# Kernel tuning notes

Hardware: AMD Instinct MI355X
Metric: run time of the kernel (lower is better)

Reference implementation:

```python
import jax, jax.numpy as jnp
import numpy as np


def setup_inputs() -> dict:
    key = jax.random.key(0)
    k1, k2 = jax.random.split(key)
    n_tokens, hidden, n_experts = 16384, 3072, 64
    activations = jax.random.normal(k1, (n_tokens, hidden), dtype=jnp.float32)
    logits = jax.random.normal(k2, (n_tokens, n_experts), dtype=jnp.float32)
    capacity = 256  # int(capacity_factor * n_tokens / n_experts) with capacity_factor=1.0
    return {"activations": activations, "logits": logits, "capacity": capacity}


def reference(activations, logits, capacity):
    """Top-1 MoE gating + capacity-limited token dispatch (DeepSpeed MoEGating, top_k=1).

    Returns (moe_input, scores, expert_assignment, mapped_slots, expert_counts).
    Dispatched rows are pre-scaled by the gate score (fused scale-and-scatter).
    """
    n_tokens, hidden = activations.shape
    n_experts = logits.shape[1]

    probs = jax.nn.softmax(logits, axis=-1)                       # [T, E], fp32
    expert = jnp.argmax(logits, axis=-1)                          # [T]
    mask1 = jax.nn.one_hot(expert, n_experts, dtype=jnp.int32)    # [T, E]

    # position of each token within its chosen expert's allocation
    locations = jnp.cumsum(mask1, axis=0) - 1                     # [T, E]
    loc_s = jnp.sum(locations * mask1, axis=1)                    # [T]

    keep = loc_s < capacity                                       # capacity-based dropping
    score = jnp.take_along_axis(probs, expert[:, None], axis=1)[:, 0]
    score = jnp.where(keep, score, 0.0)

    # dispatch buffer size, padded to a multiple of 256 (matches kernel path)
    size = n_experts * capacity
    if size % 256 != 0:
        size = size + (256 - size % 256)

    slots = expert * capacity + loc_s                             # [T]
    slots_scatter = jnp.where(keep, slots, size)                  # OOB index -> dropped

    moe_input = jnp.zeros((size, hidden), dtype=activations.dtype)
    moe_input = moe_input.at[slots_scatter].set(
        activations * score[:, None].astype(activations.dtype), mode="drop")

    expert_assignment = expert.astype(jnp.int32)
    mapped_slots = jnp.where(keep, slots, -1).astype(jnp.int32)
    expert_counts = jnp.sum(mask1 * keep[:, None].astype(jnp.int32), axis=0).astype(jnp.int32)

    return moe_input, score, expert_assignment, mapped_slots, expert_counts
```

## Files before the change

kernel.cpp:

```cpp
#include <hip/hip_runtime.h>

#define T_TOKENS 16384
#define HIDDEN   3072
#define NEXP     64
#define CAP      256
#define BLK      256
#define NGB      (T_TOKENS / BLK)
#define DSIZE    (NEXP * CAP)

__global__ __launch_bounds__(BLK) void gate_kernel(
    const float* __restrict__ logits,
    int* __restrict__ expertOut, int* __restrict__ rankOut,
    float* __restrict__ scoreOut, int* __restrict__ blockCounts) {
  __shared__ int eLds[BLK];
  __shared__ int hist[NEXP];

  const int t = blockIdx.x * BLK + threadIdx.x;

  const float4* lg = (const float4*)(logits + (size_t)t * NEXP);
  float l[NEXP];
#pragma unroll
  for (int i = 0; i < NEXP / 4; ++i) {
    float4 v = lg[i];
    l[4 * i + 0] = v.x; l[4 * i + 1] = v.y;
    l[4 * i + 2] = v.z; l[4 * i + 3] = v.w;
  }

  float mx = l[0];
  int arg = 0;
#pragma unroll
  for (int i = 1; i < NEXP; ++i) {
    if (l[i] > mx) { mx = l[i]; arg = i; }
  }
  float s = 0.f;
#pragma unroll
  for (int i = 0; i < NEXP; ++i) s += __expf(l[i] - mx);
  const float score = 1.0f / s;

  eLds[threadIdx.x] = arg;
  if (threadIdx.x < NEXP) hist[threadIdx.x] = 0;
  __syncthreads();

  int r = 0;
  const int tid = (int)threadIdx.x;
  for (int j = 0; j < BLK; ++j) {
    int ej = eLds[j];
    if (j < tid && ej == arg) ++r;
  }
  atomicAdd(&hist[arg], 1);
  __syncthreads();

  expertOut[t] = arg;
  rankOut[t]   = r;
  scoreOut[t]  = score;
  if (threadIdx.x < NEXP)
    blockCounts[blockIdx.x * NEXP + threadIdx.x] = hist[threadIdx.x];
}

__global__ void scan_kernel(int* __restrict__ base, int* __restrict__ totals,
                            float* __restrict__ countsOut) {
  const int e = threadIdx.x;
  int run = 0;
  for (int b = 0; b < NGB; ++b) {
    int c = base[b * NEXP + e];
    base[b * NEXP + e] = run;
    run += c;
  }
  totals[e] = run;
  countsOut[e] = (float)min(run, CAP);
}

__global__ __launch_bounds__(BLK) void scatter_kernel(
    const float* __restrict__ act,
    const int* __restrict__ expert, const int* __restrict__ rank,
    const float* __restrict__ score,
    const int* __restrict__ base, const int* __restrict__ totals,
    float* __restrict__ moe, float* __restrict__ scoreOut,
    float* __restrict__ assignOut, float* __restrict__ slotsOut) {
  const int i = blockIdx.x;

  const int e   = expert[i];
  const int r   = rank[i];
  const int b   = i >> 8;
  const int loc = base[b * NEXP + e] + r;
  const bool keep = loc < CAP;
  const float s = score[i];

  if (threadIdx.x == 0) {
    scoreOut[i]  = keep ? s : 0.0f;
    assignOut[i] = (float)e;
    slotsOut[i]  = keep ? (float)(e * CAP + loc) : -1.0f;
  }

  if (keep) {
    const int slot = e * CAP + loc;
    const float4* src = (const float4*)(act + (size_t)i * HIDDEN);
    float4* dst = (float4*)(moe + (size_t)slot * HIDDEN);
#pragma unroll
    for (int k = threadIdx.x; k < HIDDEN / 4; k += BLK) {
      float4 v = src[k];
      v.x *= s; v.y *= s; v.z *= s; v.w *= s;
      dst[k] = v;
    }
  }

  const int se = i / CAP;
  const int sp = i & (CAP - 1);
  const int kcnt = min(totals[se], CAP);
  if (sp >= kcnt) {
    float4* dst = (float4*)(moe + (size_t)i * HIDDEN);
    const float4 z = make_float4(0.f, 0.f, 0.f, 0.f);
#pragma unroll
    for (int k = threadIdx.x; k < HIDDEN / 4; k += BLK) dst[k] = z;
  }
}

extern "C" void kernel_launch(void* const* d_in, const int* in_sizes, int n_in,
                              void* d_out, int out_size, void* d_ws, size_t ws_size,
                              hipStream_t stream) {
  const float* act    = (const float*)d_in[0];
  const float* logits = (const float*)d_in[1];

  float* out       = (float*)d_out;
  float* moe       = out;
  float* scoreOut  = out + (size_t)DSIZE * HIDDEN;
  float* assignOut = scoreOut + T_TOKENS;
  float* slotsOut  = assignOut + T_TOKENS;
  float* countsOut = slotsOut + T_TOKENS;

  int*   expert = (int*)d_ws;
  int*   rank   = expert + T_TOKENS;
  float* score  = (float*)(rank + T_TOKENS);
  int*   base   = (int*)(score + T_TOKENS);
  int*   totals = base + NGB * NEXP;

  gate_kernel<<<NGB, BLK, 0, stream>>>(logits, expert, rank, score, base);
  scan_kernel<<<1, NEXP, 0, stream>>>(base, totals, countsOut);
  scatter_kernel<<<T_TOKENS, BLK, 0, stream>>>(act, expert, rank, score, base,
                                               totals, moe, scoreOut, assignOut,
                                               slotsOut);
}
```

Measured before the change: 349.2 us.

## Use wave-ballot ranking, parallel finalize, and destination-driven gather for dispatch

Computes each token's rank within its expert using wave ballots plus per-wave counts instead of a serial scan over the block. Replaces the single-block serial prefix scan with a parallel finalize kernel that computes bases per block and emits a slot-to-token map. The dispatch kernel then iterates over destination slots, gathering and scaling source rows or zero-filling, so writes are sequential and reads are scattered. This adds workspace buffers and a redundant per-block histogram reduction.

```diff
diff --git a/kernel.cpp b/kernel.cpp
--- a/kernel.cpp
+++ b/kernel.cpp
@@ -7,15 +7,18 @@
 #define BLK      256
 #define NGB      (T_TOKENS / BLK)
 #define DSIZE    (NEXP * CAP)
+#define NW       (BLK / 64)
 
 __global__ __launch_bounds__(BLK) void gate_kernel(
     const float* __restrict__ logits,
     int* __restrict__ expertOut, int* __restrict__ rankOut,
-    float* __restrict__ scoreOut, int* __restrict__ blockCounts) {
-  __shared__ int eLds[BLK];
-  __shared__ int hist[NEXP];
+    float* __restrict__ scoreOut, int* __restrict__ histOut) {
+  __shared__ int wcnt[NW][NEXP];
 
-  const int t = blockIdx.x * BLK + threadIdx.x;
+  const int tid  = (int)threadIdx.x;
+  const int lane = tid & 63;
+  const int w    = tid >> 6;
+  const int t    = blockIdx.x * BLK + tid;
 
   const float4* lg = (const float4*)(logits + (size_t)t * NEXP);
   float l[NEXP];
@@ -29,86 +32,112 @@
   float mx = l[0];
   int arg = 0;
 #pragma unroll
-  for (int i = 1; i < NEXP; ++i) {
+  for (int i = 1; i < NEXP; ++i)
     if (l[i] > mx) { mx = l[i]; arg = i; }
-  }
   float s = 0.f;
 #pragma unroll
   for (int i = 0; i < NEXP; ++i) s += __expf(l[i] - mx);
   const float score = 1.0f / s;
 
-  eLds[threadIdx.x] = arg;
-  if (threadIdx.x < NEXP) hist[threadIdx.x] = 0;
+  ((int*)wcnt)[tid] = 0;
   __syncthreads();
 
-  int r = 0;
-  const int tid = (int)threadIdx.x;
-  for (int j = 0; j < BLK; ++j) {
-    int ej = eLds[j];
-    if (j < tid && ej == arg) ++r;
+  unsigned long long m = ~0ull;
+#pragma unroll
+  for (int b = 0; b < 6; ++b) {
+    unsigned long long bal = __ballot((arg >> b) & 1);
+    m &= ((arg >> b) & 1) ? bal : ~bal;
   }
-  atomicAdd(&hist[arg], 1);
+  const unsigned long long ltm = (1ull << lane) - 1ull;
+  const int rankInWave = __popcll(m & ltm);
+  const bool leader = (__ffsll((unsigned long long)m) - 1) == lane;
+  if (leader) wcnt[w][arg] = __popcll(m);
   __syncthreads();
+
+  int r = rankInWave;
+#pragma unroll
+  for (int w2 = 0; w2 < NW; ++w2)
+    if (w2 < w) r += wcnt[w2][arg];
 
   expertOut[t] = arg;
   rankOut[t]   = r;
   scoreOut[t]  = score;
-  if (threadIdx.x < NEXP)
-    blockCounts[blockIdx.x * NEXP + threadIdx.x] = hist[threadIdx.x];
+  if (tid < NEXP) {
+    int h = 0;
+#pragma unroll
+    for (int w2 = 0; w2 < NW; ++w2) h += wcnt[w2][tid];
+    histOut[blockIdx.x * NEXP + tid] = h;
+  }
 }
 
-__global__ void scan_kernel(int* __restrict__ base, int* __restrict__ totals,
-                            float* __restrict__ countsOut) {
-  const int e = threadIdx.x;
-  int run = 0;
-  for (int b = 0; b < NGB; ++b) {
-    int c = base[b * NEXP + e];
-    base[b * NEXP + e] = run;
-    run += c;
+__global__ __launch_bounds__(BLK) void finalize_kernel(
+    const int* __restrict__ hist, const int* __restrict__ expert,
+    const int* __restrict__ rank, const float* __restrict__ score,
+    int* __restrict__ srcmap, float* __restrict__ sscore,
+    int* __restrict__ kcnt,
+    float* __restrict__ scoreOut, float* __restrict__ assignOut,
+    float* __restrict__ slotsOut, float* __restrict__ countsOut) {
+  __shared__ int h[NGB * NEXP];
+  __shared__ int baseSh[NEXP];
+
+  const int tid = (int)threadIdx.x;
+  const int b   = (int)blockIdx.x;
+
+  for (int i = tid; i < NGB * NEXP; i += BLK) h[i] = hist[i];
+  __syncthreads();
+
+  if (tid < NEXP) {
+    int base = 0, tot = 0;
+    for (int b2 = 0; b2 < NGB; ++b2) {
+      int c = h[b2 * NEXP + tid];
+      if (b2 < b) base += c;
+      tot += c;
+    }
+    baseSh[tid] = base;
+    if (b == 0) {
+      int kc = min(tot, CAP);
+      kcnt[tid] = kc;
+      countsOut[tid] = (float)kc;
+    }
   }
-  totals[e] = run;
-  countsOut[e] = (float)min(run, CAP);
+  __syncthreads();
+
+  const int t   = b * BLK + tid;
+  const int e   = expert[t];
+  const int loc = baseSh[e] + rank[t];
+  const float s = score[t];
+  const bool keep = loc < CAP;
+
+  scoreOut[t]  = keep ? s : 0.0f;
+  assignOut[t] = (float)e;
+  slotsOut[t]  = keep ? (float)(e * CAP + loc) : -1.0f;
+  if (keep) {
+    const int slot = e * CAP + loc;
+    srcmap[slot] = t;
+    sscore[slot] = s;
+  }
 }
 
 __global__ __launch_bounds__(BLK) void scatter_kernel(
-    const float* __restrict__ act,
-    const int* __restrict__ expert, const int* __restrict__ rank,
-    const float* __restrict__ score,
-    const int* __restrict__ base, const int* __restrict__ totals,
-    float* __restrict__ moe, float* __restrict__ scoreOut,
-    float* __restrict__ assignOut, float* __restrict__ slotsOut) {
-  const int i = blockIdx.x;
+    const float* __restrict__ act, const int* __restrict__ srcmap,
+    const float* __restrict__ sscore, const int* __restrict__ kcnt,
+    float* __restrict__ moe) {
+  const int i   = (int)blockIdx.x;
+  const int e   = i >> 8;
+  const int pos = i & (CAP - 1);
 
-  const int e   = expert[i];
-  const int r   = rank[i];
-  const int b   = i >> 8;
-  const int loc = base[b * NEXP + e] + r;
-  const bool keep = loc < CAP;
-  const float s = score[i];
-
-  if (threadIdx.x == 0) {
-    scoreOut[i]  = keep ? s : 0.0f;
-    assignOut[i] = (float)e;
-    slotsOut[i]  = keep ? (float)(e * CAP + loc) : -1.0f;
-  }
-
-  if (keep) {
-    const int slot = e * CAP + loc;
-    const float4* src = (const float4*)(act + (size_t)i * HIDDEN);
-    float4* dst = (float4*)(moe + (size_t)slot * HIDDEN);
+  float4* dst = (float4*)(moe + (size_t)i * HIDDEN);
+  if (pos < kcnt[e]) {
+    const int t   = srcmap[i];
+    const float s = sscore[i];
+    const float4* src = (const float4*)(act + (size_t)t * HIDDEN);
 #pragma unroll
     for (int k = threadIdx.x; k < HIDDEN / 4; k += BLK) {
       float4 v = src[k];
       v.x *= s; v.y *= s; v.z *= s; v.w *= s;
       dst[k] = v;
     }
-  }
-
-  const int se = i / CAP;
-  const int sp = i & (CAP - 1);
-  const int kcnt = min(totals[se], CAP);
-  if (sp >= kcnt) {
-    float4* dst = (float4*)(moe + (size_t)i * HIDDEN);
+  } else {
     const float4 z = make_float4(0.f, 0.f, 0.f, 0.f);
 #pragma unroll
     for (int k = threadIdx.x; k < HIDDEN / 4; k += BLK) dst[k] = z;
@@ -131,12 +160,15 @@
   int*   expert = (int*)d_ws;
   int*   rank   = expert + T_TOKENS;
   float* score  = (float*)(rank + T_TOKENS);
-  int*   base   = (int*)(score + T_TOKENS);
-  int*   totals = base + NGB * NEXP;
+  int*   hist   = (int*)(score + T_TOKENS);
+  int*   kcnt   = hist + NGB * NEXP;
+  int*   srcmap = kcnt + NEXP;
+  float* sscore = (float*)(srcmap + DSIZE);
 
-  gate_kernel<<<NGB, BLK, 0, stream>>>(logits, expert, rank, score, base);
-  scan_kernel<<<1, NEXP, 0, stream>>>(base, totals, countsOut);
-  scatter_kernel<<<T_TOKENS, BLK, 0, stream>>>(act, expert, rank, score, base,
-                                               totals, moe, scoreOut, assignOut,
-                                               slotsOut);
+  gate_kernel<<<NGB, BLK, 0, stream>>>(logits, expert, rank, score, hist);
+  finalize_kernel<<<NGB, BLK, 0, stream>>>(hist, expert, rank, score,
+                                           srcmap, sscore, kcnt,
+                                           scoreOut, assignOut, slotsOut,
+                                           countsOut);
+  scatter_kernel<<<DSIZE, BLK, 0, stream>>>(act, srcmap, sscore, kcnt, moe);
 }
```

Result: no change. 351.8 us (+0.7%).
